# Optimization experiments

Hardware: AMD Instinct MI355X
Metric: run time of the kernel (lower is better)

## Reference

```python
import jax, jax.numpy as jnp
import numpy as np

B, S, DIM = 2, 2048, 2048
QH, KVH = 32, 8
HD = DIM // QH            # 64
KV_DIM = HD * KVH         # 512
MAX_LEN = 2048
SCALE = HD ** -0.5
NEG_INF = -1e30


def _rope_cache(seq_len, head_dim, max_len, theta=10000.0, factor=8.0):
    # faithful to generate_sin_cos_pos_emb (causal branch, offset=0),
    # cache built at max_len then sliced to seq_len by the caller
    idx = np.arange(0, head_dim, 2, dtype=np.float64) / head_dim
    inv_freq = 1.0 / theta ** idx
    if factor > 1.0:
        seq_eff = max(max_len, max_len)  # generate called with seq_len=max_length
        adj = (factor * seq_eff / max_len - (factor - 1.0)) ** (head_dim / (head_dim - 2.0))
        inv_freq = 1.0 / (theta * adj) ** idx
    pos = np.arange(0, max_len, dtype=np.float64)
    freqs = np.einsum('i,j->ij', pos, inv_freq)
    emb = np.concatenate([freqs, freqs], axis=-1)  # [max_len, head_dim]
    cos = jnp.asarray(np.cos(emb)[:seq_len], dtype=jnp.float32)
    sin = jnp.asarray(np.sin(emb)[:seq_len], dtype=jnp.float32)
    return cos, sin


def _rotate_half(x):
    x1, x2 = jnp.split(x, 2, axis=-1)
    return jnp.concatenate([-x2, x1], axis=-1)


def _apply_rope(x, cos, sin):
    # x: [B, H, S, D]; cos/sin: [S, D]
    return x * cos + _rotate_half(x) * sin


def setup_inputs() -> dict:
    key = jax.random.key(0)
    ks = jax.random.split(key, 11)
    s = 0.02
    return {
        'query': jax.random.normal(ks[0], (B, S, DIM), jnp.float32),
        'key':   jax.random.normal(ks[1], (B, S, DIM), jnp.float32),
        'value': jax.random.normal(ks[2], (B, S, DIM), jnp.float32),
        'w_q': jax.random.normal(ks[3], (DIM, DIM), jnp.float32) * s,
        'b_q': jnp.zeros((DIM,), jnp.float32),
        'w_k': jax.random.normal(ks[4], (DIM, KV_DIM), jnp.float32) * s,
        'b_k': jnp.zeros((KV_DIM,), jnp.float32),
        'w_v': jax.random.normal(ks[5], (DIM, KV_DIM), jnp.float32) * s,
        'b_v': jnp.zeros((KV_DIM,), jnp.float32),
        'w_o': jax.random.normal(ks[6], (DIM, DIM), jnp.float32) * s,
        'b_o': jnp.zeros((DIM,), jnp.float32),
    }


def reference(query, key, value, w_q, b_q, w_k, b_k, w_v, b_v, w_o, b_o):
    # projections (weights stored as [in, out])
    q = query @ w_q + b_q                                    # [B,S,DIM]
    k = key   @ w_k + b_k                                    # [B,S,KV_DIM]
    v = value @ w_v + b_v                                    # [B,S,KV_DIM]

    q = q.reshape(B, S, QH, HD).transpose(0, 2, 1, 3)        # [B,QH,S,HD]
    k = k.reshape(B, S, KVH, HD).transpose(0, 2, 1, 3)       # [B,KVH,S,HD]
    v = v.reshape(B, S, KVH, HD).transpose(0, 2, 1, 3)       # [B,KVH,S,HD]

    cos, sin = _rope_cache(S, HD, MAX_LEN)
    q = _apply_rope(q, cos, sin)
    k = _apply_rope(k, cos, sin)

    # GQA: group queries per kv head (equivalent to repeat_interleave on K/V)
    G = QH // KVH
    qg = q.reshape(B, KVH, G, S, HD)
    scores = jnp.einsum('bhgqd,bhkd->bhgqk', qg, k) * SCALE  # [B,KVH,G,S,S]
    causal = jnp.tril(jnp.ones((S, S), dtype=bool))
    scores = jnp.where(causal, scores, NEG_INF)
    probs = jax.nn.softmax(scores, axis=-1)
    ctx = jnp.einsum('bhgqk,bhkd->bhgqd', probs, v)          # [B,KVH,G,S,HD]
    ctx = ctx.reshape(B, QH, S, HD).transpose(0, 2, 1, 3).reshape(B, S, DIM)
    return ctx @ w_o + b_o                                   # [B,S,DIM]
```

## Files before the change

kernel.cpp:

```cpp
#include <hip/hip_runtime.h>
#include <hip/hip_bf16.h>

typedef __hip_bfloat16 bf16_t;
typedef __attribute__((ext_vector_type(8))) short bf16x8;
typedef __attribute__((ext_vector_type(4))) float f32x4;

#define S_LEN   2048
#define D_MODEL 2048
#define N_QH    32
#define N_KVH   8
#define HEAD_D  64
#define KV_D    512
#define M_ROWS  4096
#define QK_SCALE (0.125f * 1.44269504088896340736f)
#define NQT     16

struct __align__(8) bf16x4s { bf16_t x, y, z, w; };

__global__ void prep_kernel(const float* __restrict__ wq, const float* __restrict__ wk,
                            const float* __restrict__ wv, const float* __restrict__ wo,
                            bf16_t* __restrict__ tq, bf16_t* __restrict__ tk,
                            bf16_t* __restrict__ tv, bf16_t* __restrict__ to,
                            const float* __restrict__ query, const float* __restrict__ key_,
                            const float* __restrict__ value,
                            bf16_t* __restrict__ qbf, bf16_t* __restrict__ kbf,
                            bf16_t* __restrict__ vbf,
                            float* __restrict__ cosT, float* __restrict__ sinT) {
    const int bx = blockIdx.x, t = threadIdx.x;
    if (bx < 10240) {
        __shared__ float tile[32][33];
        const float* W; bf16_t* Wt; int N, nb, kt;
        if (bx < 4096)      { W = wq; Wt = tq; N = D_MODEL; nb = bx & 63;          kt = bx >> 6; }
        else if (bx < 5120) { int i = bx - 4096; W = wk; Wt = tk; N = KV_D; nb = i & 15; kt = i >> 4; }
        else if (bx < 6144) { int i = bx - 5120; W = wv; Wt = tv; N = KV_D; nb = i & 15; kt = i >> 4; }
        else                { int i = bx - 6144; W = wo; Wt = to; N = D_MODEL; nb = i & 63; kt = i >> 6; }
        const int K = D_MODEL;
        int n0 = nb * 32, k0 = kt * 32;
        int tx = t & 31, ty = t >> 5;
#pragma unroll
        for (int i = 0; i < 4; i++) {
            int r = ty + i * 8;
            tile[r][tx] = W[(size_t)(k0 + r) * N + n0 + tx];
        }
        __syncthreads();
#pragma unroll
        for (int i = 0; i < 4; i++) {
            int r = ty + i * 8;
            Wt[(size_t)(n0 + r) * K + k0 + tx] = __float2bfloat16(tile[tx][r]);
        }
        return;
    }
    if (bx < 10304) {
        int blk = bx - 10240;
        int j = t & 31;
        double invf = pow(10000.0, -(double)(2 * j) / 64.0);
#pragma unroll
        for (int i = 0; i < 4; i++) {
            int pos = blk * 32 + i * 8 + (t >> 5);
            double a = (double)pos * invf;
            cosT[pos * 32 + j] = (float)cos(a);
            sinT[pos * 32 + j] = (float)sin(a);
        }
        return;
    }
    const int per = M_ROWS * D_MODEL / 4;
    int tid = (bx - 10304) * 256 + t;
    for (int i = tid; i < 3 * per; i += 1536 * 256) {
        const float* src; bf16_t* dst; int off;
        if (i < per)          { src = query; dst = qbf; off = i; }
        else if (i < 2 * per) { src = key_;  dst = kbf; off = i - per; }
        else                  { src = value; dst = vbf; off = i - 2 * per; }
        float4 v = ((const float4*)src)[off];
        bf16x4s o;
        o.x = __float2bfloat16(v.x);
        o.y = __float2bfloat16(v.y);
        o.z = __float2bfloat16(v.z);
        o.w = __float2bfloat16(v.w);
        ((bf16x4s*)dst)[off] = o;
    }
}

__device__ __forceinline__ void async_copy16(const bf16_t* g, bf16_t* l) {
    __builtin_amdgcn_global_load_lds((const __attribute__((address_space(1))) void*)g,
                                     (__attribute__((address_space(3))) void*)l, 16, 0, 0);
}

template <int ROPE, int OUTF32, int QSCALE>
__global__ __launch_bounds__(256, 2)
void gqa_gemm_kernel(const bf16_t* __restrict__ A, const bf16_t* __restrict__ Bt,
                     const float* __restrict__ bias, void* __restrict__ Cout,
                     int M, int N, int K,
                     const float* __restrict__ cosT, const float* __restrict__ sinT) {
    __shared__ __align__(16) bf16_t As[128 * 64];
    __shared__ __align__(16) bf16_t Bs[128 * 64];

    const int t = threadIdx.x;
    const int bx = blockIdx.x;
    const int xcd = bx & 7, j = bx >> 3;
    const int am0 = (((xcd >> 1) << 3) + (j >> 3)) * 128;
    const int bn0 = (((xcd & 1) << 3) + (j & 7)) * 128;

    const int l = t & 63, w = t >> 6;
    const int wr = w >> 1, wc = w & 1;
    const int lr = l & 15, lk = l >> 4;

    f32x4 acc[4][4];
#pragma unroll
    for (int i = 0; i < 4; i++)
#pragma unroll
        for (int jx = 0; jx < 4; jx++) acc[i][jx] = (f32x4)0.0f;

    const int r0 = t >> 3;
    const int c  = (t & 7) ^ (r0 & 7);
    const bf16_t* aptr = A + (size_t)(am0 + r0) * K + c * 8;
    const bf16_t* bptr = Bt + (size_t)(bn0 + r0) * K + c * 8;
    bf16_t* aLds = As + r0 * 64 + (t & 7) * 8;
    bf16_t* bLds = Bs + r0 * 64 + (t & 7) * 8;

    for (int k0 = 0; k0 < K; k0 += 64) {
#pragma unroll
        for (int s = 0; s < 4; ++s) {
            async_copy16(aptr + (size_t)(s * 32) * K + k0, aLds + s * 2048);
            async_copy16(bptr + (size_t)(s * 32) * K + k0, bLds + s * 2048);
        }
        __syncthreads();

        bf16x8 af[4][2], bfr[4][2];
#pragma unroll
        for (int mi = 0; mi < 4; mi++)
#pragma unroll
            for (int ks = 0; ks < 2; ks++)
                af[mi][ks] = *(const bf16x8*)&As[(wr * 64 + mi * 16 + lr) * 64 +
                                 ((ks * 32 + lk * 8) ^ ((lr & 7) << 3))];
#pragma unroll
        for (int ni = 0; ni < 4; ni++)
#pragma unroll
            for (int ks = 0; ks < 2; ks++)
                bfr[ni][ks] = *(const bf16x8*)&Bs[(wc * 64 + ni * 16 + lr) * 64 +
                                  ((ks * 32 + lk * 8) ^ ((lr & 7) << 3))];
#pragma unroll
        for (int mi = 0; mi < 4; mi++)
#pragma unroll
            for (int ni = 0; ni < 4; ni++)
#pragma unroll
                for (int ks = 0; ks < 2; ks++)
                    acc[mi][ni] = __builtin_amdgcn_mfma_f32_16x16x32_bf16(
                        af[mi][ks], bfr[ni][ks], acc[mi][ni], 0, 0, 0);
        __syncthreads();
    }

#pragma unroll
    for (int mi = 0; mi < 4; mi++) {
#pragma unroll
        for (int reg = 0; reg < 4; reg++) {
            int row = am0 + wr * 64 + mi * 16 + lk * 4 + reg;
            if (OUTF32) {
                float* out = (float*)Cout;
#pragma unroll
                for (int ni = 0; ni < 4; ni++) {
                    int col = bn0 + wc * 64 + ni * 16 + lr;
                    out[(size_t)row * N + col] = acc[mi][ni][reg] + bias[col];
                }
            } else if (ROPE) {
                bf16_t* out = (bf16_t*)Cout;
                int pos = row & (S_LEN - 1);
#pragma unroll
                for (int np = 0; np < 2; np++) {
                    int jj = np * 16 + lr;
                    float cs = cosT[pos * 32 + jj];
                    float sn = sinT[pos * 32 + jj];
                    int col1 = bn0 + wc * 64 + np * 16 + lr;
                    float x1 = acc[mi][np][reg] + bias[col1];
                    float x2 = acc[mi][np + 2][reg] + bias[col1 + 32];
                    float o1 = x1 * cs - x2 * sn;
                    float o2 = x2 * cs + x1 * sn;
                    if (QSCALE) { o1 *= QK_SCALE; o2 *= QK_SCALE; }
                    out[(size_t)row * N + col1]      = __float2bfloat16(o1);
                    out[(size_t)row * N + col1 + 32] = __float2bfloat16(o2);
                }
            } else {
                bf16_t* out = (bf16_t*)Cout;
#pragma unroll
                for (int ni = 0; ni < 4; ni++) {
                    int col = bn0 + wc * 64 + ni * 16 + lr;
                    out[(size_t)row * N + col] =
                        __float2bfloat16(acc[mi][ni][reg] + bias[col]);
                }
            }
        }
    }
}

__global__ __launch_bounds__(256, 2)
void gqa_qkv_kernel(const bf16_t* __restrict__ Qbf, const bf16_t* __restrict__ Kbf,
                    const bf16_t* __restrict__ Vbf,
                    const bf16_t* __restrict__ Wtq, const bf16_t* __restrict__ Wtk,
                    const bf16_t* __restrict__ Wtv,
                    const float* __restrict__ bq, const float* __restrict__ bk,
                    const float* __restrict__ bv,
                    bf16_t* __restrict__ Qout, bf16_t* __restrict__ Kout,
                    bf16_t* __restrict__ VtOut,
                    const float* __restrict__ cosT, const float* __restrict__ sinT) {
    __shared__ __align__(16) char smem[128 * 140 * 2];
    bf16_t* As = (bf16_t*)smem;
    bf16_t* Bs = (bf16_t*)(smem + 16384);
    bf16_t* TT = (bf16_t*)smem;

    const int t = threadIdx.x, bx = blockIdx.x;
    constexpr int K = D_MODEL;

    int am0, bn0, mode;
    const bf16_t *A, *Bt; const float* bias;
    if (bx < 512) {
        int xcd = bx & 7, j = bx >> 3;
        am0 = (((xcd >> 1) << 3) + (j >> 3)) * 128;
        bn0 = (((xcd & 1) << 3) + (j & 7)) * 128;
        A = Qbf; Bt = Wtq; bias = bq; mode = 0;
    } else {
        int idx = bx - 512;
        int z = idx >> 7;
        int xcd = idx & 7, jj = (idx & 127) >> 3;
        am0 = (xcd * 4 + (jj & 3)) * 128;
        bn0 = (jj >> 2) * 128;
        A = z ? Vbf : Kbf; Bt = z ? Wtv : Wtk; bias = z ? bv : bk; mode = z ? 2 : 1;
    }

    const int l = t & 63, w = t >> 6;
    const int wr = w >> 1, wc = w & 1;
    const int lr = l & 15, lk = l >> 4;

    f32x4 acc[4][4];
#pragma unroll
    for (int i = 0; i < 4; i++)
#pragma unroll
        for (int jx = 0; jx < 4; jx++) acc[i][jx] = (f32x4)0.0f;

    const int r0 = t >> 3;
    const int c  = (t & 7) ^ (r0 & 7);
    const bf16_t* aptr = A + (size_t)(am0 + r0) * K + c * 8;
    const bf16_t* bptr = Bt + (size_t)(bn0 + r0) * K + c * 8;
    bf16_t* aLds = As + r0 * 64 + (t & 7) * 8;
    bf16_t* bLds = Bs + r0 * 64 + (t & 7) * 8;

    for (int k0 = 0; k0 < K; k0 += 64) {
#pragma unroll
        for (int s = 0; s < 4; ++s) {
            async_copy16(aptr + (size_t)(s * 32) * K + k0, aLds + s * 2048);
            async_copy16(bptr + (size_t)(s * 32) * K + k0, bLds + s * 2048);
        }
        __syncthreads();

        bf16x8 af[4][2], bfr[4][2];
#pragma unroll
        for (int mi = 0; mi < 4; mi++)
#pragma unroll
            for (int ks = 0; ks < 2; ks++)
                af[mi][ks] = *(const bf16x8*)&As[(wr * 64 + mi * 16 + lr) * 64 +
                                 ((ks * 32 + lk * 8) ^ ((lr & 7) << 3))];
#pragma unroll
        for (int ni = 0; ni < 4; ni++)
#pragma unroll
            for (int ks = 0; ks < 2; ks++)
                bfr[ni][ks] = *(const bf16x8*)&Bs[(wc * 64 + ni * 16 + lr) * 64 +
                                  ((ks * 32 + lk * 8) ^ ((lr & 7) << 3))];
#pragma unroll
        for (int mi = 0; mi < 4; mi++)
#pragma unroll
            for (int ni = 0; ni < 4; ni++)
#pragma unroll
                for (int ks = 0; ks < 2; ks++)
                    acc[mi][ni] = __builtin_amdgcn_mfma_f32_16x16x32_bf16(
                        af[mi][ks], bfr[ni][ks], acc[mi][ni], 0, 0, 0);
        __syncthreads();
    }

    if (mode == 2) {
#pragma unroll
        for (int mi = 0; mi < 4; mi++)
#pragma unroll
            for (int ni = 0; ni < 4; ni++) {
                int colL = wc * 64 + ni * 16 + lr;
                float bz = bias[bn0 + colL];
                bf16x4s pk;
                pk.x = __float2bfloat16(acc[mi][ni][0] + bz);
                pk.y = __float2bfloat16(acc[mi][ni][1] + bz);
                pk.z = __float2bfloat16(acc[mi][ni][2] + bz);
                pk.w = __float2bfloat16(acc[mi][ni][3] + bz);
                *(bf16x4s*)&TT[colL * 140 + wr * 64 + mi * 16 + lk * 4] = pk;
            }
        __syncthreads();
        const int colL = t >> 1, s0 = (t & 1) * 64;
        const int cg = bn0 + colL;
        const int bI = am0 >> 11;
        bf16_t* dst = VtOut + ((size_t)(bI * N_KVH + (cg >> 6)) * HEAD_D + (cg & 63)) * S_LEN
                      + (am0 & (S_LEN - 1)) + s0;
        const bf16_t* src = &TT[colL * 140 + s0];
#pragma unroll
        for (int i = 0; i < 8; i++)
            *(bf16x8*)(dst + i * 8) = *(const bf16x8*)(src + i * 8);
        return;
    }

    const int N = (mode == 0) ? D_MODEL : KV_D;
    bf16_t* out = (mode == 0) ? Qout : Kout;
    const float qs = (mode == 0) ? QK_SCALE : 1.0f;
#pragma unroll
    for (int mi = 0; mi < 4; mi++)
#pragma unroll
        for (int reg = 0; reg < 4; reg++) {
            int row = am0 + wr * 64 + mi * 16 + lk * 4 + reg;
            int pos = row & (S_LEN - 1);
#pragma unroll
            for (int np = 0; np < 2; np++) {
                int jj = np * 16 + lr;
                float cs = cosT[pos * 32 + jj];
                float sn = sinT[pos * 32 + jj];
                int col1 = bn0 + wc * 64 + np * 16 + lr;
                float x1 = acc[mi][np][reg] + bias[col1];
                float x2 = acc[mi][np + 2][reg] + bias[col1 + 32];
                out[(size_t)row * N + col1]      = __float2bfloat16((x1 * cs - x2 * sn) * qs);
                out[(size_t)row * N + col1 + 32] = __float2bfloat16((x2 * cs + x1 * sn) * qs);
            }
        }
}

__device__ __forceinline__ void stage_K8(const bf16_t* KB, bf16_t* dst, int kt, int t) {
    const int skey = t >> 3;
    const int c    = (t & 7) ^ (skey & 7);
    async_copy16(KB + (size_t)(kt * 64 + skey) * KV_D + c * 8, dst + t * 8);
}
__device__ __forceinline__ void stage_V8(const bf16_t* VTb, bf16_t* dst, int kt, int t) {
    const int sd = t >> 3;
    const int c  = (t & 7) ^ (sd & 7);
    async_copy16(VTb + (size_t)sd * S_LEN + kt * 64 + c * 8, dst + t * 8);
}

__global__ __launch_bounds__(512, 4)
void gqa_attn_kernel(const bf16_t* __restrict__ Q, const bf16_t* __restrict__ Kb,
                     const bf16_t* __restrict__ VT, bf16_t* __restrict__ Ctx) {
    __shared__ __align__(16) bf16_t Ks[2][64 * 64];
    __shared__ __align__(16) bf16_t Vs[2][64 * 64];
    __shared__ __align__(16) bf16_t Pw[8][16 * 72];

    const int t = threadIdx.x, l = t & 63, w = t >> 6;
    const int lr = l & 15, lk = l >> 4;

    const int flat = blockIdx.x;
    const int xcd = flat & 7, j0 = flat >> 3;
    const int qt  = NQT - 1 - (j0 >> 3);
    const int rem = j0 & 7;
    const int combo = xcd * 2 + (rem >> 2);
    const int b   = combo >> 3;
    const int kvh = combo & 7;
    const int h   = kvh * 4 + (rem & 3);

    bf16x8 vones;
#pragma unroll
    for (int i = 0; i < 8; i++) vones[i] = (short)0x3F80;

    const bf16_t* KB  = Kb + (size_t)b * S_LEN * KV_D + kvh * HEAD_D;
    const bf16_t* VTb = VT + ((size_t)(b * N_KVH + kvh) * HEAD_D) * S_LEN;

    const int q0w = qt * 128 + w * 16;
    const int qg  = q0w + lr;

    bf16x8 qf[2];
    {
        const bf16_t* qrow = Q + ((size_t)(b * S_LEN + qg)) * D_MODEL + h * HEAD_D;
        qf[0] = *(const bf16x8*)(qrow + lk * 8);
        qf[1] = *(const bf16x8*)(qrow + 32 + lk * 8);
    }

    f32x4 oaccT[4];
    f32x4 oaccS = (f32x4)0.0f;
#pragma unroll
    for (int df = 0; df < 4; df++) oaccT[df] = (f32x4)0.0f;

    const int nkt = 2 * qt + 2;

    stage_K8(KB, Ks[0], 0, t);
    stage_V8(VTb, Vs[0], 0, t);
    __syncthreads();

    int cur = 0;
    for (int kt = 0; kt < nkt; ++kt) {
        const bool pre = (kt + 1 < nkt);
        if (pre) {
            stage_K8(KB, Ks[cur ^ 1], kt + 1, t);
            stage_V8(VTb, Vs[cur ^ 1], kt + 1, t);
        }

        if (kt * 64 <= q0w + 15) {
            const bool diag = (kt * 64 + 63 > q0w);

            f32x4 sfrT[4];
#pragma unroll
            for (int ni = 0; ni < 4; ni++) sfrT[ni] = (f32x4)0.0f;
            __builtin_amdgcn_s_setprio(1);
#pragma unroll
            for (int ni = 0; ni < 4; ni++)
#pragma unroll
                for (int ks = 0; ks < 2; ks++) {
                    bf16x8 kf = *(const bf16x8*)&Ks[cur][(ni * 16 + lr) * 64 +
                                    ((ks * 32 + lk * 8) ^ ((lr & 7) << 3))];
                    sfrT[ni] = __builtin_amdgcn_mfma_f32_16x16x32_bf16(kf, qf[ks],
                                                                       sfrT[ni], 0, 0, 0);
                }
            __builtin_amdgcn_s_setprio(0);

#pragma unroll
            for (int ni = 0; ni < 4; ni++) {
                float sc0 = sfrT[ni][0], sc1 = sfrT[ni][1];
                float sc2 = sfrT[ni][2], sc3 = sfrT[ni][3];
                if (diag) {
                    int kbase = kt * 64 + ni * 16 + lk * 4;
                    if (kbase + 0 > qg) sc0 = -1e30f;
                    if (kbase + 1 > qg) sc1 = -1e30f;
                    if (kbase + 2 > qg) sc2 = -1e30f;
                    if (kbase + 3 > qg) sc3 = -1e30f;
                }
                bf16x4s pk;
                pk.x = __float2bfloat16(exp2f(sc0));
                pk.y = __float2bfloat16(exp2f(sc1));
                pk.z = __float2bfloat16(exp2f(sc2));
                pk.w = __float2bfloat16(exp2f(sc3));
                *(bf16x4s*)&Pw[w][lr * 72 + ni * 16 + lk * 4] = pk;
            }

            __builtin_amdgcn_s_setprio(1);
#pragma unroll
            for (int ks = 0; ks < 2; ks++) {
                bf16x8 pf = *(const bf16x8*)&Pw[w][lr * 72 + ks * 32 + lk * 8];
                oaccS = __builtin_amdgcn_mfma_f32_16x16x32_bf16(vones, pf, oaccS, 0, 0, 0);
#pragma unroll
                for (int df = 0; df < 4; df++) {
                    bf16x8 vf = *(const bf16x8*)&Vs[cur][(df * 16 + lr) * 64 +
                                    ((ks * 32 + lk * 8) ^ ((lr & 7) << 3))];
                    oaccT[df] = __builtin_amdgcn_mfma_f32_16x16x32_bf16(vf, pf,
                                        oaccT[df], 0, 0, 0);
                }
            }
            __builtin_amdgcn_s_setprio(0);
        }

        __syncthreads();
        cur ^= 1;
    }

    {
        float inv = 1.0f / oaccS[0];
        bf16_t* crow = Ctx + ((size_t)(b * S_LEN + qg)) * D_MODEL + h * HEAD_D;
#pragma unroll
        for (int df = 0; df < 4; df++) {
            bf16x4s ov;
            ov.x = __float2bfloat16(oaccT[df][0] * inv);
            ov.y = __float2bfloat16(oaccT[df][1] * inv);
            ov.z = __float2bfloat16(oaccT[df][2] * inv);
            ov.w = __float2bfloat16(oaccT[df][3] * inv);
            *(bf16x4s*)(crow + df * 16 + lk * 4) = ov;
        }
    }
}

extern "C" void kernel_launch(void* const* d_in, const int* in_sizes, int n_in,
                              void* d_out, int out_size, void* d_ws, size_t ws_size,
                              hipStream_t stream) {
    const float* query = (const float*)d_in[0];
    const float* key_  = (const float*)d_in[1];
    const float* value = (const float*)d_in[2];
    const float* w_q = (const float*)d_in[3];
    const float* b_q = (const float*)d_in[4];
    const float* w_k = (const float*)d_in[5];
    const float* b_k = (const float*)d_in[6];
    const float* w_v = (const float*)d_in[7];
    const float* b_v = (const float*)d_in[8];
    const float* w_o = (const float*)d_in[9];
    const float* b_o = (const float*)d_in[10];
    float* out = (float*)d_out;

    char* ws = (char*)d_ws;
    bf16_t* qbf  = (bf16_t*)(ws);
    bf16_t* qb   = (bf16_t*)(ws + (size_t)(16 << 20));
    bf16_t* kb   = (bf16_t*)(ws + (size_t)(32 << 20));
    bf16_t* vt   = (bf16_t*)(ws + (size_t)(36 << 20));
    bf16_t* wtq  = (bf16_t*)(ws + (size_t)(40 << 20));
    bf16_t* wtk  = (bf16_t*)(ws + (size_t)(48 << 20));
    bf16_t* wtv  = (bf16_t*)(ws + (size_t)(50 << 20));
    bf16_t* wto  = (bf16_t*)(ws + (size_t)(52 << 20));
    float* cosT  = (float*)(ws + (size_t)(60 << 20));
    float* sinT  = (float*)(ws + (size_t)(60 << 20) + (256 << 10));
    bf16_t* kbf  = (bf16_t*)(ws + (size_t)(61 << 20));
    bf16_t* vbf  = (bf16_t*)(ws + (size_t)(77 << 20));

    prep_kernel<<<11840, 256, 0, stream>>>(w_q, w_k, w_v, w_o, wtq, wtk, wtv, wto,
                                           query, key_, value, qbf, kbf, vbf, cosT, sinT);

    gqa_qkv_kernel<<<768, 256, 0, stream>>>(qbf, kbf, vbf, wtq, wtk, wtv,
                                            b_q, b_k, b_v, qb, kb, vt, cosT, sinT);

    gqa_attn_kernel<<<1024, 512, 0, stream>>>(qb, kb, vt, qbf);

    gqa_gemm_kernel<0, 1, 0><<<512, 256, 0, stream>>>(
        qbf, wto, b_o, out, M_ROWS, D_MODEL, D_MODEL, cosT, sinT);
}
```

Before: 204.3 us.

## Load V fragments directly from global and triple-buffer K in LDS

V is no longer staged through shared memory. Each wave loads its V MFMA fragments straight from global memory into registers at the start of every key tile. K moves to a three-slot LDS ring that prefetches two tiles ahead, and the block-wide sync is replaced by a manual vmcnt wait plus a raw s_barrier. The goal is to cut LDS traffic and barrier stalls and to hide K latency better. In exchange, all eight waves now fetch the same V tile from global/L2, and the vmcnt(1) accounting near the end of the loop may not guarantee the last staged K tile has landed.

```diff
diff --git a/kernel.cpp b/kernel.cpp
--- a/kernel.cpp
+++ b/kernel.cpp
@@ -329,17 +329,11 @@
     const int c    = (t & 7) ^ (skey & 7);
     async_copy16(KB + (size_t)(kt * 64 + skey) * KV_D + c * 8, dst + t * 8);
 }
-__device__ __forceinline__ void stage_V8(const bf16_t* VTb, bf16_t* dst, int kt, int t) {
-    const int sd = t >> 3;
-    const int c  = (t & 7) ^ (sd & 7);
-    async_copy16(VTb + (size_t)sd * S_LEN + kt * 64 + c * 8, dst + t * 8);
-}
 
 __global__ __launch_bounds__(512, 4)
 void gqa_attn_kernel(const bf16_t* __restrict__ Q, const bf16_t* __restrict__ Kb,
                      const bf16_t* __restrict__ VT, bf16_t* __restrict__ Ctx) {
-    __shared__ __align__(16) bf16_t Ks[2][64 * 64];
-    __shared__ __align__(16) bf16_t Vs[2][64 * 64];
+    __shared__ __align__(16) bf16_t Ks[3][64 * 64];
     __shared__ __align__(16) bf16_t Pw[8][16 * 72];
 
     const int t = threadIdx.x, l = t & 63, w = t >> 6;
@@ -379,18 +373,27 @@
     const int nkt = 2 * qt + 2;
 
     stage_K8(KB, Ks[0], 0, t);
-    stage_V8(VTb, Vs[0], 0, t);
+    stage_K8(KB, Ks[1], 1, t);
     __syncthreads();
 
-    int cur = 0;
     for (int kt = 0; kt < nkt; ++kt) {
-        const bool pre = (kt + 1 < nkt);
-        if (pre) {
-            stage_K8(KB, Ks[cur ^ 1], kt + 1, t);
-            stage_V8(VTb, Vs[cur ^ 1], kt + 1, t);
-        }
-
-        if (kt * 64 <= q0w + 15) {
+        const int cur = kt % 3;
+        const bool compute = (kt * 64 <= q0w + 15);
+
+        bf16x8 vfr[2][4];
+        if (compute) {
+#pragma unroll
+            for (int ks = 0; ks < 2; ks++)
+#pragma unroll
+                for (int df = 0; df < 4; df++)
+                    vfr[ks][df] = *(const bf16x8*)&VTb[(size_t)(df * 16 + lr) * S_LEN +
+                                                       kt * 64 + ks * 32 + lk * 8];
+        }
+        if (kt + 2 < nkt)
+            stage_K8(KB, Ks[(kt + 2) % 3], kt + 2, t);
+        __builtin_amdgcn_sched_barrier(0);
+
+        if (compute) {
             const bool diag = (kt * 64 + 63 > q0w);
 
             f32x4 sfrT[4];
@@ -433,18 +436,20 @@
                 bf16x8 pf = *(const bf16x8*)&Pw[w][lr * 72 + ks * 32 + lk * 8];
                 oaccS = __builtin_amdgcn_mfma_f32_16x16x32_bf16(vones, pf, oaccS, 0, 0, 0);
 #pragma unroll
-                for (int df = 0; df < 4; df++) {
-                    bf16x8 vf = *(const bf16x8*)&Vs[cur][(df * 16 + lr) * 64 +
-                                    ((ks * 32 + lk * 8) ^ ((lr & 7) << 3))];
-                    oaccT[df] = __builtin_amdgcn_mfma_f32_16x16x32_bf16(vf, pf,
+                for (int df = 0; df < 4; df++)
+                    oaccT[df] = __builtin_amdgcn_mfma_f32_16x16x32_bf16(vfr[ks][df], pf,
                                         oaccT[df], 0, 0, 0);
-                }
             }
             __builtin_amdgcn_s_setprio(0);
         }
 
-        __syncthreads();
-        cur ^= 1;
+        if (kt + 1 < nkt) {
+            __builtin_amdgcn_sched_barrier(0);
+            asm volatile("s_waitcnt vmcnt(1)" ::: "memory");
+        }
+        __builtin_amdgcn_sched_barrier(0);
+        __builtin_amdgcn_s_barrier();
+        __builtin_amdgcn_sched_barrier(0);
     }
 
     {
```

New measurement: 267.6 us. +31.0%, slower.
